# Optimization experiments

Measured on AMD Instinct MI355X. Metric: run time of the kernel, lower is better.

## Reference

```python
import jax, jax.numpy as jnp
import numpy as np

ALPHA = 0.2  # LeakyReLU negative slope
NEG_INF = -1.0e9

def gat_layer(h, adj_mask, W, a, concat):
    # h: [B,N,Fin], W: [Fout,Fin] (torch Linear layout), a: [2*Fout]
    Wh = jnp.einsum('bni,oi->bno', h, W)  # [B,N,Fout]
    F_out = W.shape[0]
    # a([Wh_i, Wh_j]) = Wh_i . a[:F] + Wh_j . a[F:]  (avoids O(N^2*2F) concat, same math)
    s_src = Wh @ a[:F_out]  # [B,N]
    s_dst = Wh @ a[F_out:]  # [B,N]
    e = jax.nn.leaky_relu(s_src[:, :, None] + s_dst[:, None, :], ALPHA)  # [B,N,N]
    e = jnp.where(adj_mask, e, NEG_INF)
    att = jax.nn.softmax(e, axis=-1)  # dropout is identity in eval mode
    h_prime = jnp.einsum('bij,bjf->bif', att, Wh)
    return jax.nn.elu(h_prime) if concat else h_prime

def setup_inputs() -> dict:
    key = jax.random.key(0)
    ks = jax.random.split(key, 8)
    B, N = 4, 2048
    IN, HID, OUT, H = 64, 64, 32, 4
    x = jax.random.normal(ks[0], (B, N, IN), dtype=jnp.float32)
    adj = jax.random.randint(ks[1], (B, N, N), 0, 2, dtype=jnp.int32)

    def xavier(k, shape):
        fan_out, fan_in = shape[0], shape[1]
        lim = float(np.sqrt(6.0 / (fan_in + fan_out)))
        return jax.random.uniform(k, shape, jnp.float32, -lim, lim)

    W1 = jnp.stack([xavier(jax.random.fold_in(ks[2], i), (HID, IN)) for i in range(H)])      # [H,64,64]
    a1 = jnp.stack([xavier(jax.random.fold_in(ks[3], i), (1, 2 * HID))[0] for i in range(H)])  # [H,128]
    W2 = xavier(ks[4], (OUT, H * HID))  # [32,256]
    a2 = xavier(ks[5], (1, 2 * OUT))[0]  # [64]
    return {"x": x, "adj": adj, "W1": W1, "a1": a1, "W2": W2, "a2": a2}

def reference(x, adj, W1, a1, W2, a2):
    mask = adj > 0
    # layer 1: num_heads concat heads with ELU
    heads = [gat_layer(x, mask, W1[k], a1[k], True) for k in range(W1.shape[0])]
    h = jnp.concatenate(heads, axis=-1)  # [B,N,H*HID]
    # output layer: single head, no ELU
    return gat_layer(h, mask, W2, a2, False)
```

## Files before the change

### kernel.cpp

```cpp
#include <hip/hip_runtime.h>
#include <hip/hip_bf16.h>
#include <cstdint>

#define NN 2048
#define NH 4
#define NW 64

typedef __attribute__((ext_vector_type(8))) short bf16x8;
typedef __attribute__((ext_vector_type(4))) float f32x4;
typedef __attribute__((ext_vector_type(4))) int i32x4;
typedef __attribute__((ext_vector_type(4))) unsigned short u16x4;

__device__ __forceinline__ float lrelu(float s) { return s > 0.f ? s : 0.2f * s; }

__device__ __forceinline__ unsigned pk2(float lo, float hi) {
  __hip_bfloat162 h2 = __float22bfloat162_rn(make_float2(lo, hi));
  union { __hip_bfloat162 h; unsigned u; } c; c.h = h2; return c.u;
}
__device__ __forceinline__ unsigned short f2bf1(float f) {
  __hip_bfloat16 h = __float2bfloat16(f);
  union { __hip_bfloat16 h; unsigned short u; } c; c.h = h; return c.u;
}
__device__ __forceinline__ bf16x8 cvt8(f32x4 v0, f32x4 v1) {
  union { unsigned u[4]; bf16x8 v; } r;
  r.u[0] = pk2(v0[0], v0[1]); r.u[1] = pk2(v0[2], v0[3]);
  r.u[2] = pk2(v1[0], v1[1]); r.u[3] = pk2(v1[2], v1[3]);
  return r.v;
}


__global__ __launch_bounds__(256) void kA(
    const int* __restrict__ adj, unsigned* __restrict__ mb,
    const float* __restrict__ x, const float* __restrict__ W1,
    const float* __restrict__ a1, unsigned short* __restrict__ wht1,
    float* __restrict__ ssrc1, float* __restrict__ G1g, float* __restrict__ G2g) {
  if (blockIdx.x >= 512) {
    size_t gid = (size_t)(blockIdx.x - 512) * 256 + threadIdx.x;
    const i32x4* ap = (const i32x4*)adj + gid * 8;
    i32x4 v0 = __builtin_nontemporal_load(ap + 0);
    i32x4 v1 = __builtin_nontemporal_load(ap + 1);
    i32x4 v2 = __builtin_nontemporal_load(ap + 2);
    i32x4 v3 = __builtin_nontemporal_load(ap + 3);
    i32x4 v4 = __builtin_nontemporal_load(ap + 4);
    i32x4 v5 = __builtin_nontemporal_load(ap + 5);
    i32x4 v6 = __builtin_nontemporal_load(ap + 6);
    i32x4 v7 = __builtin_nontemporal_load(ap + 7);
    unsigned word = 0;
#pragma unroll
    for (int j = 0; j < 4; ++j) {
      word |= ((unsigned)(v0[j] != 0)) << (0 + j);
      word |= ((unsigned)(v1[j] != 0)) << (4 + j);
      word |= ((unsigned)(v2[j] != 0)) << (8 + j);
      word |= ((unsigned)(v3[j] != 0)) << (12 + j);
      word |= ((unsigned)(v4[j] != 0)) << (16 + j);
      word |= ((unsigned)(v5[j] != 0)) << (20 + j);
      word |= ((unsigned)(v6[j] != 0)) << (24 + j);
      word |= ((unsigned)(v7[j] != 0)) << (28 + j);
    }
    mb[gid] = word;
    return;
  }
  int blk = blockIdx.x;
  int rowg = blk * 16;
  int b = rowg >> 11, rloc = rowg & (NN - 1);
  int tid = threadIdx.x, lane = tid & 63, h = tid >> 6;
  int cl = lane & 15, g = lane >> 4;

  const float* xr = x + (size_t)(rowg + cl) * 64 + 8 * g;
  bf16x8 af[2];
#pragma unroll
  for (int ks = 0; ks < 2; ++ks)
    af[ks] = cvt8(*(const f32x4*)(xr + ks * 32), *(const f32x4*)(xr + ks * 32 + 4));

  f32x4 zero = {0.f, 0.f, 0.f, 0.f};
  f32x4 acc[4] = {zero, zero, zero, zero};
#pragma unroll
  for (int ft = 0; ft < 4; ++ft) {
    const float* wr = W1 + (size_t)(h * 64 + ft * 16 + cl) * 64 + 8 * g;
#pragma unroll
    for (int ks = 0; ks < 2; ++ks) {
      bf16x8 bfr = cvt8(*(const f32x4*)(wr + ks * 32), *(const f32x4*)(wr + ks * 32 + 4));
      acc[ft] = __builtin_amdgcn_mfma_f32_16x16x32_bf16(af[ks], bfr, acc[ft], 0, 0, 0);
    }
  }
  unsigned short* bhb = wht1 + (size_t)(b * NH + h) * 64 * NN;
  int kb = rloc >> 5;
  int gd = ((rloc >> 3) & 2) + (g >> 1);
  int e0 = 4 * (g & 1);
  float ps[4] = {0.f, 0.f, 0.f, 0.f}, pd[4] = {0.f, 0.f, 0.f, 0.f};
#pragma unroll
  for (int ft = 0; ft < 4; ++ft) {
    float as = a1[h * 128 + ft * 16 + cl];
    float ad = a1[h * 128 + 64 + ft * 16 + cl];
    u16x4 w4;
#pragma unroll
    for (int r = 0; r < 4; ++r) {
      float v = acc[ft][r];
      w4[r] = f2bf1(v);
      ps[r] += v * as; pd[r] += v * ad;
    }
    *(u16x4*)(bhb + (size_t)(kb * 4 + ft) * 512 + cl * 8 + gd * 128 + e0) = w4;
  }
#pragma unroll
  for (int r = 0; r < 4; ++r) {
    float s = ps[r], d = pd[r];
    s += __shfl_xor(s, 1); s += __shfl_xor(s, 2); s += __shfl_xor(s, 4); s += __shfl_xor(s, 8);
    d += __shfl_xor(d, 1); d += __shfl_xor(d, 2); d += __shfl_xor(d, 4); d += __shfl_xor(d, 8);
    if (cl == 0) {
      int idx = (b * NH + h) * NN + rloc + 4 * g + r;
      ssrc1[idx] = s;
      G1g[idx] = __expf(d);
      G2g[idx] = __expf(0.2f * d);
    }
  }
}

__global__ __launch_bounds__(512) void k2_attn1(
    const unsigned short* __restrict__ wht1, const float* __restrict__ ssrc1,
    const float* __restrict__ G1g, const float* __restrict__ G2g,
    const unsigned* __restrict__ mb, unsigned short* __restrict__ hout) {
  __shared__ __align__(16) char smem[33280];
  __shared__ float swmax[8];
  unsigned (*sdm)[65] = (unsigned(*)[65])smem;
  float* sG1 = (float*)(smem + 16640);
  float* sG2 = (float*)(smem + 16640 + 8192);
  float (*cmb)[16][68] = (float(*)[16][68])smem;
  float (*sden)[16] = (float(*)[16])(smem + 17408);

  int bid = blockIdx.x;
  int bh = bid & 15, tile = bid >> 4;
  int b = bh >> 2, h = bh & 3;
  int rowblk = tile << 6;
  int t = threadIdx.x, lane = t & 63, w = t >> 6;
  int wloc = w & 3, jh = w >> 2;
  int cl = lane & 15, g = lane >> 4, g8 = g * 8;

  {
    int row = t >> 3, c = (t & 7) * 8;
    const unsigned* mrow = mb + (size_t)(b * NN + rowblk + row) * NW + c;
    uint4 v0 = *(const uint4*)(mrow);
    uint4 v1 = *(const uint4*)(mrow + 4);
    sdm[row][c + 0] = v0.x; sdm[row][c + 1] = v0.y;
    sdm[row][c + 2] = v0.z; sdm[row][c + 3] = v0.w;
    sdm[row][c + 4] = v1.x; sdm[row][c + 5] = v1.y;
    sdm[row][c + 6] = v1.z; sdm[row][c + 7] = v1.w;
  }
  {
    const f32x4* g1p = (const f32x4*)(G1g + (size_t)(b * NH + h) * NN);
    const f32x4* g2p = (const f32x4*)(G2g + (size_t)(b * NH + h) * NN);
    f32x4 gv = g1p[t];
    ((f32x4*)sG1)[t] = gv;
    ((f32x4*)sG2)[t] = g2p[t];
    float gmx = fmaxf(fmaxf(gv[0], gv[1]), fmaxf(gv[2], gv[3]));
    gmx = fmaxf(gmx, __shfl_xor(gmx, 1));  gmx = fmaxf(gmx, __shfl_xor(gmx, 2));
    gmx = fmaxf(gmx, __shfl_xor(gmx, 4));  gmx = fmaxf(gmx, __shfl_xor(gmx, 8));
    gmx = fmaxf(gmx, __shfl_xor(gmx, 16)); gmx = fmaxf(gmx, __shfl_xor(gmx, 32));
    if (lane == 0) swmax[w] = gmx;
  }
  int rowW = rowblk + wloc * 16;
  float s = ssrc1[(size_t)(b * NH + h) * NN + rowW + cl];
  __syncthreads();
  float mxv = fmaxf(fmaxf(fmaxf(swmax[0], swmax[1]), fmaxf(swmax[2], swmax[3])),
                    fmaxf(fmaxf(swmax[4], swmax[5]), fmaxf(swmax[6], swmax[7])));
  float logMx = __logf(mxv);
  float m = lrelu(s + logMx);
  float F1 = __expf(s - m), F2 = __expf(0.2f * s - m);

  short onev = (cl == 0) ? (short)0x3F80 : (short)0;
  bf16x8 ones = {onev, onev, onev, onev, onev, onev, onev, onev};
  f32x4 zero = {0.f, 0.f, 0.f, 0.f};
  f32x4 acc[4] = {zero, zero, zero, zero};
  f32x4 acc1 = zero;
  const unsigned short* fbase = wht1 + (size_t)(b * NH + h) * 64 * NN + lane * 8;
  int rloc = wloc * 16 + cl;
  int kb0 = jh * 32;

  bf16x8 curf[4], nxtf[4];
#pragma unroll
  for (int ft = 0; ft < 4; ++ft)
    curf[ft] = *(const bf16x8*)(fbase + (size_t)(kb0 * 4 + ft) * 512);

  for (int i = 0; i < 32; ++i) {
    int kb = kb0 + i;
    if (i < 31) {
#pragma unroll
      for (int ft = 0; ft < 4; ++ft)
        nxtf[ft] = *(const bf16x8*)(fbase + (size_t)((kb + 1) * 4 + ft) * 512);
    }
    unsigned by = (sdm[rloc][kb] >> g8) & 0xFFu;
    int j0 = kb * 32 + g8;
    f32x4 g1a = *(const f32x4*)(sG1 + j0);
    f32x4 g1b = *(const f32x4*)(sG1 + j0 + 4);
    f32x4 g2a = *(const f32x4*)(sG2 + j0);
    f32x4 g2b = *(const f32x4*)(sG2 + j0 + 4);
    float wv[8];
#pragma unroll
    for (int e = 0; e < 8; ++e) {
      float g1 = (e < 4) ? g1a[e] : g1b[e - 4];
      float g2 = (e < 4) ? g2a[e] : g2b[e - 4];
      float v = fmaxf(F1 * g1, F2 * g2);
      wv[e] = ((by >> e) & 1u) ? v : 0.f;
    }
    union { unsigned u[4]; bf16x8 v; } pa;
    pa.u[0] = pk2(wv[0], wv[1]); pa.u[1] = pk2(wv[2], wv[3]);
    pa.u[2] = pk2(wv[4], wv[5]); pa.u[3] = pk2(wv[6], wv[7]);
#pragma unroll
    for (int ft = 0; ft < 4; ++ft)
      acc[ft] = __builtin_amdgcn_mfma_f32_16x16x32_bf16(pa.v, curf[ft], acc[ft], 0, 0, 0);
    acc1 = __builtin_amdgcn_mfma_f32_16x16x32_bf16(pa.v, ones, acc1, 0, 0, 0);
#pragma unroll
    for (int ft = 0; ft < 4; ++ft) curf[ft] = nxtf[ft];
  }
  __syncthreads();
  if (jh == 1) {
#pragma unroll
    for (int ft = 0; ft < 4; ++ft)
#pragma unroll
      for (int r = 0; r < 4; ++r)
        cmb[wloc][4 * g + r][ft * 16 + cl] = acc[ft][r];
    if (cl == 0) {
#pragma unroll
      for (int r = 0; r < 4; ++r) sden[wloc][4 * g + r] = acc1[r];
    }
  }
  __syncthreads();
  if (jh == 0) {
#pragma unroll
    for (int r = 0; r < 4; ++r) {
      int rowm = 4 * g + r;
      float dself = __shfl(acc1[r], lane & 48);
      float inv = 1.f / (dself + sden[wloc][rowm]);
      unsigned short* dst = hout + (size_t)(b * NN + rowW + rowm) * 256 + h * 64;
#pragma unroll
      for (int ft = 0; ft < 4; ++ft) {
        float v = (acc[ft][r] + cmb[wloc][rowm][ft * 16 + cl]) * inv;
        v = v > 0.f ? v : (__expf(v) - 1.f);
        dst[ft * 16 + cl] = f2bf1(v);
      }
    }
  }
}

__global__ __launch_bounds__(256) void k3_proj2(
    const unsigned short* __restrict__ hin, const float* __restrict__ W2,
    const float* __restrict__ a2, unsigned short* __restrict__ wh2t,
    float* __restrict__ ssrc2, float* __restrict__ G1o, float* __restrict__ G2o) {
  __shared__ float cmb[4][16][33];
  int blk = blockIdx.x;
  int b = blk >> 7, rowbase = (blk & 127) << 4;
  int t = threadIdx.x, lane = t & 63, w = t >> 6;
  int cl = lane & 15, g = lane >> 4;
  int k0 = w * 64;

  const unsigned short* hr = hin + (size_t)(b * NN + rowbase + cl) * 256 + k0 + 8 * g;
  bf16x8 af[2];
#pragma unroll
  for (int ks = 0; ks < 2; ++ks)
    af[ks] = *(const bf16x8*)(hr + ks * 32);

  f32x4 zero = {0.f, 0.f, 0.f, 0.f};
  f32x4 acc[2] = {zero, zero};
#pragma unroll
  for (int ft = 0; ft < 2; ++ft) {
    const float* wr = W2 + (size_t)(ft * 16 + cl) * 256 + k0 + 8 * g;
#pragma unroll
    for (int ks = 0; ks < 2; ++ks) {
      bf16x8 bfr = cvt8(*(const f32x4*)(wr + ks * 32), *(const f32x4*)(wr + ks * 32 + 4));
      acc[ft] = __builtin_amdgcn_mfma_f32_16x16x32_bf16(af[ks], bfr, acc[ft], 0, 0, 0);
    }
  }
#pragma unroll
  for (int ft = 0; ft < 2; ++ft)
#pragma unroll
    for (int r = 0; r < 4; ++r)
      cmb[w][4 * g + r][ft * 16 + cl] = acc[ft][r];
  __syncthreads();

  int row = t >> 4, c0 = t & 15;
  float v0 = cmb[0][row][c0] + cmb[1][row][c0] + cmb[2][row][c0] + cmb[3][row][c0];
  float v1 = cmb[0][row][c0 + 16] + cmb[1][row][c0 + 16] + cmb[2][row][c0 + 16] + cmb[3][row][c0 + 16];
  float ps = v0 * a2[c0] + v1 * a2[c0 + 16];
  float pd = v0 * a2[32 + c0] + v1 * a2[32 + c0 + 16];
  ps += __shfl_xor(ps, 1); ps += __shfl_xor(ps, 2); ps += __shfl_xor(ps, 4); ps += __shfl_xor(ps, 8);
  pd += __shfl_xor(pd, 1); pd += __shfl_xor(pd, 2); pd += __shfl_xor(pd, 4); pd += __shfl_xor(pd, 8);
  if (c0 == 0) {
    int idx = b * NN + rowbase + row;
    ssrc2[idx] = ps;
    G1o[idx] = __expf(pd);
    G2o[idx] = __expf(0.2f * pd);
  }
  cmb[0][row][c0] = v0;
  cmb[0][row][c0 + 16] = v1;
  __syncthreads();
  int col = t >> 3, rg = t & 7;
  unsigned pk = pk2(cmb[0][2 * rg][col], cmb[0][2 * rg + 1][col]);
  int kb2 = rowbase >> 5;
  int gd = ((rowbase >> 3) & 2) + (rg >> 2);
  size_t off = (size_t)(kb2 * 2 + (col >> 4)) * 512 + (col & 15) * 8 + gd * 128 + 2 * (rg & 3);
  *(unsigned*)(wh2t + (size_t)b * 32 * NN + off) = pk;
}

__global__ __launch_bounds__(512) void k4_attn2(
    const unsigned short* __restrict__ wh2t, const float* __restrict__ ssrc2,
    const float* __restrict__ G1o, const float* __restrict__ G2o,
    const unsigned* __restrict__ mb, float* __restrict__ outp) {
  __shared__ __align__(16) char smem[24704];
  __shared__ float swmax[8];
  unsigned (*sdm)[65] = (unsigned(*)[65])smem;
  float* sG1 = (float*)(smem + 8320);
  float* sG2 = (float*)(smem + 8320 + 8192);
  float (*cmb)[2][16][36] = (float(*)[2][16][36])smem;
  float (*sden)[2][16] = (float(*)[2][16])(smem + 13824);

  int bid = blockIdx.x;
  int b = bid & 3, tile = bid >> 2;
  int rowblk = tile << 5;
  int t = threadIdx.x, lane = t & 63, w = t >> 6;
  int wloc = w & 1, jh = w >> 1;
  int cl = lane & 15, g = lane >> 4, g8 = g * 8;

  {
    int row = t >> 4, c = (t & 15) * 4;
    uint4 v = *(const uint4*)(mb + (size_t)(b * NN + rowblk + row) * NW + c);
    sdm[row][c + 0] = v.x; sdm[row][c + 1] = v.y;
    sdm[row][c + 2] = v.z; sdm[row][c + 3] = v.w;
  }
  {
    f32x4 gv = ((const f32x4*)(G1o + (size_t)b * NN))[t];
    ((f32x4*)sG1)[t] = gv;
    ((f32x4*)sG2)[t] = ((const f32x4*)(G2o + (size_t)b * NN))[t];
    float gmx = fmaxf(fmaxf(gv[0], gv[1]), fmaxf(gv[2], gv[3]));
    gmx = fmaxf(gmx, __shfl_xor(gmx, 1));  gmx = fmaxf(gmx, __shfl_xor(gmx, 2));
    gmx = fmaxf(gmx, __shfl_xor(gmx, 4));  gmx = fmaxf(gmx, __shfl_xor(gmx, 8));
    gmx = fmaxf(gmx, __shfl_xor(gmx, 16)); gmx = fmaxf(gmx, __shfl_xor(gmx, 32));
    if (lane == 0) swmax[w] = gmx;
  }
  int rowW = rowblk + wloc * 16;
  float s = ssrc2[b * NN + rowW + cl];
  __syncthreads();
  float mxv = fmaxf(fmaxf(fmaxf(swmax[0], swmax[1]), fmaxf(swmax[2], swmax[3])),
                    fmaxf(fmaxf(swmax[4], swmax[5]), fmaxf(swmax[6], swmax[7])));
  float logMx = __logf(mxv);
  float m = lrelu(s + logMx);
  float F1 = __expf(s - m), F2 = __expf(0.2f * s - m);

  short onev = (cl == 0) ? (short)0x3F80 : (short)0;
  bf16x8 ones = {onev, onev, onev, onev, onev, onev, onev, onev};
  f32x4 zero = {0.f, 0.f, 0.f, 0.f};
  f32x4 acc[2] = {zero, zero};
  f32x4 acc1 = zero;
  const unsigned short* fbase = wh2t + (size_t)b * 32 * NN + lane * 8;
  int rloc = wloc * 16 + cl;
  int kb0 = jh * 16;

  bf16x8 curf[2], nxtf[2];
#pragma unroll
  for (int ft = 0; ft < 2; ++ft)
    curf[ft] = *(const bf16x8*)(fbase + (size_t)(kb0 * 2 + ft) * 512);

  for (int i = 0; i < 16; ++i) {
    int kb = kb0 + i;
    if (i < 15) {
#pragma unroll
      for (int ft = 0; ft < 2; ++ft)
        nxtf[ft] = *(const bf16x8*)(fbase + (size_t)((kb + 1) * 2 + ft) * 512);
    }
    unsigned by = (sdm[rloc][kb] >> g8) & 0xFFu;
    int j0 = kb * 32 + g8;
    f32x4 g1a = *(const f32x4*)(sG1 + j0);
    f32x4 g1b = *(const f32x4*)(sG1 + j0 + 4);
    f32x4 g2a = *(const f32x4*)(sG2 + j0);
    f32x4 g2b = *(const f32x4*)(sG2 + j0 + 4);
    float wv[8];
#pragma unroll
    for (int e = 0; e < 8; ++e) {
      float g1 = (e < 4) ? g1a[e] : g1b[e - 4];
      float g2 = (e < 4) ? g2a[e] : g2b[e - 4];
      float v = fmaxf(F1 * g1, F2 * g2);
      wv[e] = ((by >> e) & 1u) ? v : 0.f;
    }
    union { unsigned u[4]; bf16x8 v; } pa;
    pa.u[0] = pk2(wv[0], wv[1]); pa.u[1] = pk2(wv[2], wv[3]);
    pa.u[2] = pk2(wv[4], wv[5]); pa.u[3] = pk2(wv[6], wv[7]);
#pragma unroll
    for (int ft = 0; ft < 2; ++ft)
      acc[ft] = __builtin_amdgcn_mfma_f32_16x16x32_bf16(pa.v, curf[ft], acc[ft], 0, 0, 0);
    acc1 = __builtin_amdgcn_mfma_f32_16x16x32_bf16(pa.v, ones, acc1, 0, 0, 0);
#pragma unroll
    for (int ft = 0; ft < 2; ++ft) curf[ft] = nxtf[ft];
  }
  __syncthreads();
  if (jh > 0) {
#pragma unroll
    for (int ft = 0; ft < 2; ++ft)
#pragma unroll
      for (int r = 0; r < 4; ++r)
        cmb[jh - 1][wloc][4 * g + r][ft * 16 + cl] = acc[ft][r];
    if (cl == 0) {
#pragma unroll
      for (int r = 0; r < 4; ++r) sden[jh - 1][wloc][4 * g + r] = acc1[r];
    }
  }
  __syncthreads();
  if (jh == 0) {
#pragma unroll
    for (int r = 0; r < 4; ++r) {
      int rowm = 4 * g + r;
      float dself = __shfl(acc1[r], lane & 48);
      float den = dself + sden[0][wloc][rowm] + sden[1][wloc][rowm] + sden[2][wloc][rowm];
      float inv = 1.f / den;
      float* dst = outp + (size_t)(b * NN + rowW + rowm) * 32;
#pragma unroll
      for (int ft = 0; ft < 2; ++ft) {
        float v = acc[ft][r] + cmb[0][wloc][rowm][ft * 16 + cl] +
                  cmb[1][wloc][rowm][ft * 16 + cl] + cmb[2][wloc][rowm][ft * 16 + cl];
        dst[ft * 16 + cl] = v * inv;
      }
    }
  }
}

extern "C" void kernel_launch(void* const* d_in, const int* in_sizes, int n_in,
                              void* d_out, int out_size, void* d_ws, size_t ws_size,
                              hipStream_t stream) {
  (void)in_sizes; (void)n_in; (void)out_size; (void)ws_size;
  const float* x   = (const float*)d_in[0];
  const int*   adj = (const int*)d_in[1];
  const float* W1  = (const float*)d_in[2];
  const float* a1  = (const float*)d_in[3];
  const float* W2  = (const float*)d_in[4];
  const float* a2  = (const float*)d_in[5];
  float* outp = (float*)d_out;
  char* ws = (char*)d_ws;

  unsigned*       mbits = (unsigned*)(ws);
  unsigned short* wht1  = (unsigned short*)(ws + (size_t)(2u << 20));
  float*          ssrc1 = (float*)(ws + (size_t)(6u << 20));
  float*          G1g   = (float*)(ws + (size_t)(6u << 20) + (128u << 10));
  float*          G2g   = (float*)(ws + (size_t)(6u << 20) + (256u << 10));
  unsigned short* hbuf  = (unsigned short*)(ws + (size_t)(6u << 20) + (512u << 10));
  unsigned short* wh2t  = (unsigned short*)(ws + (size_t)(14u << 20) + (512u << 10));
  float*          ssrc2 = (float*)(ws + (size_t)(15u << 20));
  float*          G1o   = (float*)(ws + (size_t)(15u << 20) + (32u << 10));
  float*          G2o   = (float*)(ws + (size_t)(15u << 20) + (64u << 10));

  kA      <<<2560, 256, 0, stream>>>(adj, mbits, x, W1, a1, wht1, ssrc1, G1g, G2g);
  k2_attn1<<<512,  512, 0, stream>>>(wht1, ssrc1, G1g, G2g, mbits, hbuf);
  k3_proj2<<<512,  256, 0, stream>>>(hbuf, W2, a2, wh2t, ssrc2, G1o, G2o);
  k4_attn2<<<256,  512, 0, stream>>>(wh2t, ssrc2, G1o, G2o, mbits, outp);
}
```

Measured before the change: 165.9 us.

## Reorganize attn1 warps to 2 row-tiles x 4 K-splits, reusing B fragments

The layer-1 attention kernel now assigns each wave 32 rows (two 16-row MFMA tiles) and splits the neighbour dimension four ways instead of two. Each loaded Wh fragment therefore feeds two MFMAs, halving the global B-operand traffic per wave and shortening each wave's loop. The cost is a larger shared buffer for reducing three partial accumulators, more registers per wave, and a launch_bounds occupancy hint of 4 blocks. The larger LDS footprint may limit how many blocks fit per CU.

```diff
diff --git a/kernel.cpp b/kernel.cpp
--- a/kernel.cpp
+++ b/kernel.cpp
@@ -115,25 +115,26 @@
   }
 }
 
-__global__ __launch_bounds__(512) void k2_attn1(
+__global__ __launch_bounds__(512, 4) void k2_attn1(
     const unsigned short* __restrict__ wht1, const float* __restrict__ ssrc1,
     const float* __restrict__ G1g, const float* __restrict__ G2g,
     const unsigned* __restrict__ mb, unsigned short* __restrict__ hout) {
-  __shared__ __align__(16) char smem[33280];
+  __shared__ __align__(16) char smem[53248];
   __shared__ float swmax[8];
   unsigned (*sdm)[65] = (unsigned(*)[65])smem;
   float* sG1 = (float*)(smem + 16640);
   float* sG2 = (float*)(smem + 16640 + 8192);
-  float (*cmb)[16][68] = (float(*)[16][68])smem;
-  float (*sden)[16] = (float(*)[16])(smem + 17408);
+  float (*cmb)[2][32][68] = (float(*)[2][32][68])smem;
+  float (*sden)[2][32] = (float(*)[2][32])(smem + 52224);
 
   int bid = blockIdx.x;
   int bh = bid & 15, tile = bid >> 4;
   int b = bh >> 2, h = bh & 3;
   int rowblk = tile << 6;
   int t = threadIdx.x, lane = t & 63, w = t >> 6;
-  int wloc = w & 3, jh = w >> 2;
+  int rt = w & 1, jh = w >> 1;
   int cl = lane & 15, g = lane >> 4, g8 = g * 8;
+  int rbase = rt * 32;
 
   {
     int row = t >> 3, c = (t & 7) * 8;
@@ -157,85 +158,105 @@
     gmx = fmaxf(gmx, __shfl_xor(gmx, 16)); gmx = fmaxf(gmx, __shfl_xor(gmx, 32));
     if (lane == 0) swmax[w] = gmx;
   }
-  int rowW = rowblk + wloc * 16;
-  float s = ssrc1[(size_t)(b * NH + h) * NN + rowW + cl];
+  size_t sbase = (size_t)(b * NH + h) * NN + rowblk + rbase;
+  float s0 = ssrc1[sbase + cl];
+  float s1 = ssrc1[sbase + 16 + cl];
   __syncthreads();
   float mxv = fmaxf(fmaxf(fmaxf(swmax[0], swmax[1]), fmaxf(swmax[2], swmax[3])),
                     fmaxf(fmaxf(swmax[4], swmax[5]), fmaxf(swmax[6], swmax[7])));
   float logMx = __logf(mxv);
-  float m = lrelu(s + logMx);
-  float F1 = __expf(s - m), F2 = __expf(0.2f * s - m);
+  float m0 = lrelu(s0 + logMx), m1 = lrelu(s1 + logMx);
+  float F10 = __expf(s0 - m0), F20 = __expf(0.2f * s0 - m0);
+  float F11 = __expf(s1 - m1), F21 = __expf(0.2f * s1 - m1);
 
   short onev = (cl == 0) ? (short)0x3F80 : (short)0;
   bf16x8 ones = {onev, onev, onev, onev, onev, onev, onev, onev};
   f32x4 zero = {0.f, 0.f, 0.f, 0.f};
-  f32x4 acc[4] = {zero, zero, zero, zero};
-  f32x4 acc1 = zero;
+  f32x4 acc[2][4] = {{zero, zero, zero, zero}, {zero, zero, zero, zero}};
+  f32x4 accd[2] = {zero, zero};
   const unsigned short* fbase = wht1 + (size_t)(b * NH + h) * 64 * NN + lane * 8;
-  int rloc = wloc * 16 + cl;
-  int kb0 = jh * 32;
+  int kb0 = jh * 16;
 
   bf16x8 curf[4], nxtf[4];
 #pragma unroll
   for (int ft = 0; ft < 4; ++ft)
     curf[ft] = *(const bf16x8*)(fbase + (size_t)(kb0 * 4 + ft) * 512);
 
-  for (int i = 0; i < 32; ++i) {
+  for (int i = 0; i < 16; ++i) {
     int kb = kb0 + i;
-    if (i < 31) {
+    if (i < 15) {
 #pragma unroll
       for (int ft = 0; ft < 4; ++ft)
         nxtf[ft] = *(const bf16x8*)(fbase + (size_t)((kb + 1) * 4 + ft) * 512);
     }
-    unsigned by = (sdm[rloc][kb] >> g8) & 0xFFu;
+    unsigned by0 = (sdm[rbase + cl][kb] >> g8) & 0xFFu;
+    unsigned by1 = (sdm[rbase + 16 + cl][kb] >> g8) & 0xFFu;
     int j0 = kb * 32 + g8;
     f32x4 g1a = *(const f32x4*)(sG1 + j0);
     f32x4 g1b = *(const f32x4*)(sG1 + j0 + 4);
     f32x4 g2a = *(const f32x4*)(sG2 + j0);
     f32x4 g2b = *(const f32x4*)(sG2 + j0 + 4);
-    float wv[8];
+    float wv0[8], wv1[8];
 #pragma unroll
     for (int e = 0; e < 8; ++e) {
       float g1 = (e < 4) ? g1a[e] : g1b[e - 4];
       float g2 = (e < 4) ? g2a[e] : g2b[e - 4];
-      float v = fmaxf(F1 * g1, F2 * g2);
-      wv[e] = ((by >> e) & 1u) ? v : 0.f;
-    }
-    union { unsigned u[4]; bf16x8 v; } pa;
-    pa.u[0] = pk2(wv[0], wv[1]); pa.u[1] = pk2(wv[2], wv[3]);
-    pa.u[2] = pk2(wv[4], wv[5]); pa.u[3] = pk2(wv[6], wv[7]);
-#pragma unroll
-    for (int ft = 0; ft < 4; ++ft)
-      acc[ft] = __builtin_amdgcn_mfma_f32_16x16x32_bf16(pa.v, curf[ft], acc[ft], 0, 0, 0);
-    acc1 = __builtin_amdgcn_mfma_f32_16x16x32_bf16(pa.v, ones, acc1, 0, 0, 0);
+      float v0 = fmaxf(F10 * g1, F20 * g2);
+      float v1 = fmaxf(F11 * g1, F21 * g2);
+      wv0[e] = ((by0 >> e) & 1u) ? v0 : 0.f;
+      wv1[e] = ((by1 >> e) & 1u) ? v1 : 0.f;
+    }
+    union { unsigned u[4]; bf16x8 v; } pa0, pa1;
+    pa0.u[0] = pk2(wv0[0], wv0[1]); pa0.u[1] = pk2(wv0[2], wv0[3]);
+    pa0.u[2] = pk2(wv0[4], wv0[5]); pa0.u[3] = pk2(wv0[6], wv0[7]);
+    pa1.u[0] = pk2(wv1[0], wv1[1]); pa1.u[1] = pk2(wv1[2], wv1[3]);
+    pa1.u[2] = pk2(wv1[4], wv1[5]); pa1.u[3] = pk2(wv1[6], wv1[7]);
+#pragma unroll
+    for (int ft = 0; ft < 4; ++ft) {
+      acc[0][ft] = __builtin_amdgcn_mfma_f32_16x16x32_bf16(pa0.v, curf[ft], acc[0][ft], 0, 0, 0);
+      acc[1][ft] = __builtin_amdgcn_mfma_f32_16x16x32_bf16(pa1.v, curf[ft], acc[1][ft], 0, 0, 0);
+    }
+    accd[0] = __builtin_amdgcn_mfma_f32_16x16x32_bf16(pa0.v, ones, accd[0], 0, 0, 0);
+    accd[1] = __builtin_amdgcn_mfma_f32_16x16x32_bf16(pa1.v, ones, accd[1], 0, 0, 0);
 #pragma unroll
     for (int ft = 0; ft < 4; ++ft) curf[ft] = nxtf[ft];
   }
   __syncthreads();
-  if (jh == 1) {
-#pragma unroll
-    for (int ft = 0; ft < 4; ++ft)
-#pragma unroll
-      for (int r = 0; r < 4; ++r)
-        cmb[wloc][4 * g + r][ft * 16 + cl] = acc[ft][r];
-    if (cl == 0) {
-#pragma unroll
-      for (int r = 0; r < 4; ++r) sden[wloc][4 * g + r] = acc1[r];
+  if (jh > 0) {
+    int p = jh - 1;
+#pragma unroll
+    for (int f = 0; f < 2; ++f) {
+#pragma unroll
+      for (int ft = 0; ft < 4; ++ft)
+#pragma unroll
+        for (int r = 0; r < 4; ++r)
+          cmb[p][rt][f * 16 + 4 * g + r][ft * 16 + cl] = acc[f][ft][r];
+      if (cl == 0) {
+#pragma unroll
+        for (int r = 0; r < 4; ++r) sden[p][rt][f * 16 + 4 * g + r] = accd[f][r];
+      }
     }
   }
   __syncthreads();
   if (jh == 0) {
 #pragma unroll
-    for (int r = 0; r < 4; ++r) {
-      int rowm = 4 * g + r;
-      float dself = __shfl(acc1[r], lane & 48);
-      float inv = 1.f / (dself + sden[wloc][rowm]);
-      unsigned short* dst = hout + (size_t)(b * NN + rowW + rowm) * 256 + h * 64;
-#pragma unroll
-      for (int ft = 0; ft < 4; ++ft) {
-        float v = (acc[ft][r] + cmb[wloc][rowm][ft * 16 + cl]) * inv;
-        v = v > 0.f ? v : (__expf(v) - 1.f);
-        dst[ft * 16 + cl] = f2bf1(v);
+    for (int f = 0; f < 2; ++f) {
+#pragma unroll
+      for (int r = 0; r < 4; ++r) {
+        int rloc32 = f * 16 + 4 * g + r;
+        float dself = __shfl(accd[f][r], lane & 48);
+        float den = dself + sden[0][rt][rloc32] + sden[1][rt][rloc32] + sden[2][rt][rloc32];
+        float inv = 1.f / den;
+        int row = rowblk + rbase + rloc32;
+        unsigned short* dst = hout + (size_t)(b * NN + row) * 256 + h * 64;
+#pragma unroll
+        for (int ft = 0; ft < 4; ++ft) {
+          float v = acc[f][ft][r] + cmb[0][rt][rloc32][ft * 16 + cl] +
+                    cmb[1][rt][rloc32][ft * 16 + cl] + cmb[2][rt][rloc32][ft * 16 + cl];
+          v *= inv;
+          v = v > 0.f ? v : (__expf(v) - 1.f);
+          dst[ft * 16 + cl] = f2bf1(v);
+        }
       }
     }
   }
```

New measurement: 164.8 us. Within noise of the previous version (-0.6%).

## Fuse adjacency bitmask packing into layer-1 attention and retile attention kernels

Applied to the files above, without the earlier changes.

Moves the int32 adjacency-to-bitmask conversion out of the projection kernel and into the layer-1 attention kernel. Each block now handles 16 rows for all 4 heads, so the adjacency is read once, packed straight into shared memory, and also written out for layer 2. This avoids writing the bitmask and reading it back within layer 1. Layer-2 attention is retiled to 16 rows per block with 8 waves splitting the key range, which doubles the block count. In exchange, shared memory per layer-1 block grows to about 70KB, which may limit occupancy, and the adjacency read is now serialized before the MFMA loop instead of running concurrently with the projection work.

```diff
diff --git a/kernel.cpp b/kernel.cpp
--- a/kernel.cpp
+++ b/kernel.cpp
@@ -30,36 +30,9 @@
 
 
 __global__ __launch_bounds__(256) void kA(
-    const int* __restrict__ adj, unsigned* __restrict__ mb,
     const float* __restrict__ x, const float* __restrict__ W1,
     const float* __restrict__ a1, unsigned short* __restrict__ wht1,
     float* __restrict__ ssrc1, float* __restrict__ G1g, float* __restrict__ G2g) {
-  if (blockIdx.x >= 512) {
-    size_t gid = (size_t)(blockIdx.x - 512) * 256 + threadIdx.x;
-    const i32x4* ap = (const i32x4*)adj + gid * 8;
-    i32x4 v0 = __builtin_nontemporal_load(ap + 0);
-    i32x4 v1 = __builtin_nontemporal_load(ap + 1);
-    i32x4 v2 = __builtin_nontemporal_load(ap + 2);
-    i32x4 v3 = __builtin_nontemporal_load(ap + 3);
-    i32x4 v4 = __builtin_nontemporal_load(ap + 4);
-    i32x4 v5 = __builtin_nontemporal_load(ap + 5);
-    i32x4 v6 = __builtin_nontemporal_load(ap + 6);
-    i32x4 v7 = __builtin_nontemporal_load(ap + 7);
-    unsigned word = 0;
-#pragma unroll
-    for (int j = 0; j < 4; ++j) {
-      word |= ((unsigned)(v0[j] != 0)) << (0 + j);
-      word |= ((unsigned)(v1[j] != 0)) << (4 + j);
-      word |= ((unsigned)(v2[j] != 0)) << (8 + j);
-      word |= ((unsigned)(v3[j] != 0)) << (12 + j);
-      word |= ((unsigned)(v4[j] != 0)) << (16 + j);
-      word |= ((unsigned)(v5[j] != 0)) << (20 + j);
-      word |= ((unsigned)(v6[j] != 0)) << (24 + j);
-      word |= ((unsigned)(v7[j] != 0)) << (28 + j);
-    }
-    mb[gid] = word;
-    return;
-  }
   int blk = blockIdx.x;
   int rowg = blk * 16;
   int b = rowg >> 11, rloc = rowg & (NN - 1);
@@ -115,53 +88,80 @@
   }
 }
 
-__global__ __launch_bounds__(512) void k2_attn1(
+__global__ __launch_bounds__(512, 4) void k2_attn1(
+    const int* __restrict__ adj, unsigned* __restrict__ mb,
     const unsigned short* __restrict__ wht1, const float* __restrict__ ssrc1,
     const float* __restrict__ G1g, const float* __restrict__ G2g,
-    const unsigned* __restrict__ mb, unsigned short* __restrict__ hout) {
-  __shared__ __align__(16) char smem[33280];
+    unsigned short* __restrict__ hout) {
+  __shared__ __align__(16) char smem[69696];
   __shared__ float swmax[8];
   unsigned (*sdm)[65] = (unsigned(*)[65])smem;
-  float* sG1 = (float*)(smem + 16640);
-  float* sG2 = (float*)(smem + 16640 + 8192);
-  float (*cmb)[16][68] = (float(*)[16][68])smem;
-  float (*sden)[16] = (float(*)[16])(smem + 17408);
+  float* sG1 = (float*)(smem + 4160);
+  float* sG2 = (float*)(smem + 4160 + 32768);
+  float (*cmb)[16][68] = (float(*)[16][68])(smem + 4160);
+  float (*sden)[16] = (float(*)[16])(smem + 4160 + 17408);
 
   int bid = blockIdx.x;
-  int bh = bid & 15, tile = bid >> 4;
-  int b = bh >> 2, h = bh & 3;
-  int rowblk = tile << 6;
+  int b = bid & 3, tile = bid >> 2;
+  int rowblk = tile << 4;
   int t = threadIdx.x, lane = t & 63, w = t >> 6;
-  int wloc = w & 3, jh = w >> 2;
+  int h = w >> 1, jh = w & 1;
   int cl = lane & 15, g = lane >> 4, g8 = g * 8;
 
   {
-    int row = t >> 3, c = (t & 7) * 8;
-    const unsigned* mrow = mb + (size_t)(b * NN + rowblk + row) * NW + c;
-    uint4 v0 = *(const uint4*)(mrow);
-    uint4 v1 = *(const uint4*)(mrow + 4);
-    sdm[row][c + 0] = v0.x; sdm[row][c + 1] = v0.y;
-    sdm[row][c + 2] = v0.z; sdm[row][c + 3] = v0.w;
-    sdm[row][c + 4] = v1.x; sdm[row][c + 5] = v1.y;
-    sdm[row][c + 6] = v1.z; sdm[row][c + 7] = v1.w;
+    int r = t >> 5;
+    int w2 = (t & 31) * 2;
+    const int* arow = adj + ((size_t)(b * NN) + rowblk + r) * NN;
+    unsigned* mrow = mb + ((size_t)(b * NN) + rowblk + r) * NW;
+#pragma unroll
+    for (int k = 0; k < 2; ++k) {
+      int wd = w2 + k;
+      const i32x4* ap = (const i32x4*)(arow + wd * 32);
+      i32x4 v0 = __builtin_nontemporal_load(ap + 0);
+      i32x4 v1 = __builtin_nontemporal_load(ap + 1);
+      i32x4 v2 = __builtin_nontemporal_load(ap + 2);
+      i32x4 v3 = __builtin_nontemporal_load(ap + 3);
+      i32x4 v4 = __builtin_nontemporal_load(ap + 4);
+      i32x4 v5 = __builtin_nontemporal_load(ap + 5);
+      i32x4 v6 = __builtin_nontemporal_load(ap + 6);
+      i32x4 v7 = __builtin_nontemporal_load(ap + 7);
+      unsigned word = 0;
+#pragma unroll
+      for (int j = 0; j < 4; ++j) {
+        word |= ((unsigned)(v0[j] != 0)) << (0 + j);
+        word |= ((unsigned)(v1[j] != 0)) << (4 + j);
+        word |= ((unsigned)(v2[j] != 0)) << (8 + j);
+        word |= ((unsigned)(v3[j] != 0)) << (12 + j);
+        word |= ((unsigned)(v4[j] != 0)) << (16 + j);
+        word |= ((unsigned)(v5[j] != 0)) << (20 + j);
+        word |= ((unsigned)(v6[j] != 0)) << (24 + j);
+        word |= ((unsigned)(v7[j] != 0)) << (28 + j);
+      }
+      sdm[r][wd] = word;
+      mrow[wd] = word;
+    }
   }
   {
-    const f32x4* g1p = (const f32x4*)(G1g + (size_t)(b * NH + h) * NN);
-    const f32x4* g2p = (const f32x4*)(G2g + (size_t)(b * NH + h) * NN);
-    f32x4 gv = g1p[t];
-    ((f32x4*)sG1)[t] = gv;
-    ((f32x4*)sG2)[t] = g2p[t];
-    float gmx = fmaxf(fmaxf(gv[0], gv[1]), fmaxf(gv[2], gv[3]));
+    const f32x4* g1p = (const f32x4*)(G1g + (size_t)(b * NH + h) * NN) + jh * 256;
+    const f32x4* g2p = (const f32x4*)(G2g + (size_t)(b * NH + h) * NN) + jh * 256;
+    f32x4* d1 = (f32x4*)(sG1 + h * NN) + jh * 256;
+    f32x4* d2 = (f32x4*)(sG2 + h * NN) + jh * 256;
+    float gmx = 0.f;
+#pragma unroll
+    for (int it = 0; it < 4; ++it) {
+      f32x4 v = g1p[it * 64 + lane];
+      d1[it * 64 + lane] = v;
+      d2[it * 64 + lane] = g2p[it * 64 + lane];
+      gmx = fmaxf(fmaxf(gmx, v[0]), fmaxf(v[1], fmaxf(v[2], v[3])));
+    }
     gmx = fmaxf(gmx, __shfl_xor(gmx, 1));  gmx = fmaxf(gmx, __shfl_xor(gmx, 2));
     gmx = fmaxf(gmx, __shfl_xor(gmx, 4));  gmx = fmaxf(gmx, __shfl_xor(gmx, 8));
     gmx = fmaxf(gmx, __shfl_xor(gmx, 16)); gmx = fmaxf(gmx, __shfl_xor(gmx, 32));
     if (lane == 0) swmax[w] = gmx;
   }
-  int rowW = rowblk + wloc * 16;
-  float s = ssrc1[(size_t)(b * NH + h) * NN + rowW + cl];
-  __syncthreads();
-  float mxv = fmaxf(fmaxf(fmaxf(swmax[0], swmax[1]), fmaxf(swmax[2], swmax[3])),
-                    fmaxf(fmaxf(swmax[4], swmax[5]), fmaxf(swmax[6], swmax[7])));
+  float s = ssrc1[(size_t)(b * NH + h) * NN + rowblk + cl];
+  __syncthreads();
+  float mxv = fmaxf(swmax[h * 2], swmax[h * 2 + 1]);
   float logMx = __logf(mxv);
   float m = lrelu(s + logMx);
   float F1 = __expf(s - m), F2 = __expf(0.2f * s - m);
@@ -172,7 +172,8 @@
   f32x4 acc[4] = {zero, zero, zero, zero};
   f32x4 acc1 = zero;
   const unsigned short* fbase = wht1 + (size_t)(b * NH + h) * 64 * NN + lane * 8;
-  int rloc = wloc * 16 + cl;
+  const float* gh1 = sG1 + h * NN;
+  const float* gh2 = sG2 + h * NN;
   int kb0 = jh * 32;
 
   bf16x8 curf[4], nxtf[4];
@@ -187,12 +188,12 @@
       for (int ft = 0; ft < 4; ++ft)
         nxtf[ft] = *(const bf16x8*)(fbase + (size_t)((kb + 1) * 4 + ft) * 512);
     }
-    unsigned by = (sdm[rloc][kb] >> g8) & 0xFFu;
+    unsigned by = (sdm[cl][kb] >> g8) & 0xFFu;
     int j0 = kb * 32 + g8;
-    f32x4 g1a = *(const f32x4*)(sG1 + j0);
-    f32x4 g1b = *(const f32x4*)(sG1 + j0 + 4);
-    f32x4 g2a = *(const f32x4*)(sG2 + j0);
-    f32x4 g2b = *(const f32x4*)(sG2 + j0 + 4);
+    f32x4 g1a = *(const f32x4*)(gh1 + j0);
+    f32x4 g1b = *(const f32x4*)(gh1 + j0 + 4);
+    f32x4 g2a = *(const f32x4*)(gh2 + j0);
+    f32x4 g2b = *(const f32x4*)(gh2 + j0 + 4);
     float wv[8];
 #pragma unroll
     for (int e = 0; e < 8; ++e) {
@@ -217,10 +218,10 @@
     for (int ft = 0; ft < 4; ++ft)
 #pragma unroll
       for (int r = 0; r < 4; ++r)
-        cmb[wloc][4 * g + r][ft * 16 + cl] = acc[ft][r];
+        cmb[h][4 * g + r][ft * 16 + cl] = acc[ft][r];
     if (cl == 0) {
 #pragma unroll
-      for (int r = 0; r < 4; ++r) sden[wloc][4 * g + r] = acc1[r];
+      for (int r = 0; r < 4; ++r) sden[h][4 * g + r] = acc1[r];
     }
   }
   __syncthreads();
@@ -229,11 +230,11 @@
     for (int r = 0; r < 4; ++r) {
       int rowm = 4 * g + r;
       float dself = __shfl(acc1[r], lane & 48);
-      float inv = 1.f / (dself + sden[wloc][rowm]);
-      unsigned short* dst = hout + (size_t)(b * NN + rowW + rowm) * 256 + h * 64;
+      float inv = 1.f / (dself + sden[h][rowm]);
+      unsigned short* dst = hout + (size_t)(b * NN + rowblk + rowm) * 256 + h * 64;
 #pragma unroll
       for (int ft = 0; ft < 4; ++ft) {
-        float v = (acc[ft][r] + cmb[wloc][rowm][ft * 16 + cl]) * inv;
+        float v = (acc[ft][r] + cmb[h][rowm][ft * 16 + cl]) * inv;
         v = v > 0.f ? v : (__expf(v) - 1.f);
         dst[ft * 16 + cl] = f2bf1(v);
       }
@@ -304,26 +305,24 @@
     const unsigned short* __restrict__ wh2t, const float* __restrict__ ssrc2,
     const float* __restrict__ G1o, const float* __restrict__ G2o,
     const unsigned* __restrict__ mb, float* __restrict__ outp) {
-  __shared__ __align__(16) char smem[24704];
+  __shared__ __align__(16) char smem[20608];
   __shared__ float swmax[8];
   unsigned (*sdm)[65] = (unsigned(*)[65])smem;
-  float* sG1 = (float*)(smem + 8320);
-  float* sG2 = (float*)(smem + 8320 + 8192);
-  float (*cmb)[2][16][36] = (float(*)[2][16][36])smem;
-  float (*sden)[2][16] = (float(*)[2][16])(smem + 13824);
+  float* sG1 = (float*)(smem + 4160);
+  float* sG2 = (float*)(smem + 4160 + 8192);
+  float (*cmb)[16][36] = (float(*)[16][36])smem;
+  float (*sden)[16] = (float(*)[16])(smem + 16128);
 
   int bid = blockIdx.x;
   int b = bid & 3, tile = bid >> 2;
-  int rowblk = tile << 5;
+  int rowblk = tile << 4;
   int t = threadIdx.x, lane = t & 63, w = t >> 6;
-  int wloc = w & 1, jh = w >> 1;
   int cl = lane & 15, g = lane >> 4, g8 = g * 8;
 
   {
-    int row = t >> 4, c = (t & 15) * 4;
-    uint4 v = *(const uint4*)(mb + (size_t)(b * NN + rowblk + row) * NW + c);
+    int row = t >> 5, c = (t & 31) * 2;
+    uint2 v = *(const uint2*)(mb + (size_t)(b * NN + rowblk + row) * NW + c);
     sdm[row][c + 0] = v.x; sdm[row][c + 1] = v.y;
-    sdm[row][c + 2] = v.z; sdm[row][c + 3] = v.w;
   }
   {
     f32x4 gv = ((const f32x4*)(G1o + (size_t)b * NN))[t];
@@ -335,8 +334,7 @@
     gmx = fmaxf(gmx, __shfl_xor(gmx, 16)); gmx = fmaxf(gmx, __shfl_xor(gmx, 32));
     if (lane == 0) swmax[w] = gmx;
   }
-  int rowW = rowblk + wloc * 16;
-  float s = ssrc2[b * NN + rowW + cl];
+  float s = ssrc2[b * NN + rowblk + cl];
   __syncthreads();
   float mxv = fmaxf(fmaxf(fmaxf(swmax[0], swmax[1]), fmaxf(swmax[2], swmax[3])),
                     fmaxf(fmaxf(swmax[4], swmax[5]), fmaxf(swmax[6], swmax[7])));
@@ -350,22 +348,21 @@
   f32x4 acc[2] = {zero, zero};
   f32x4 acc1 = zero;
   const unsigned short* fbase = wh2t + (size_t)b * 32 * NN + lane * 8;
-  int rloc = wloc * 16 + cl;
-  int kb0 = jh * 16;
+  int kb0 = w * 8;
 
   bf16x8 curf[2], nxtf[2];
 #pragma unroll
   for (int ft = 0; ft < 2; ++ft)
     curf[ft] = *(const bf16x8*)(fbase + (size_t)(kb0 * 2 + ft) * 512);
 
-  for (int i = 0; i < 16; ++i) {
+  for (int i = 0; i < 8; ++i) {
     int kb = kb0 + i;
-    if (i < 15) {
+    if (i < 7) {
 #pragma unroll
       for (int ft = 0; ft < 2; ++ft)
         nxtf[ft] = *(const bf16x8*)(fbase + (size_t)((kb + 1) * 2 + ft) * 512);
     }
-    unsigned by = (sdm[rloc][kb] >> g8) & 0xFFu;
+    unsigned by = (sdm[cl][kb] >> g8) & 0xFFu;
     int j0 = kb * 32 + g8;
     f32x4 g1a = *(const f32x4*)(sG1 + j0);
     f32x4 g1b = *(const f32x4*)(sG1 + j0 + 4);
@@ -390,30 +387,34 @@
     for (int ft = 0; ft < 2; ++ft) curf[ft] = nxtf[ft];
   }
   __syncthreads();
-  if (jh > 0) {
+  if (w > 0) {
+    int p = w - 1;
 #pragma unroll
     for (int ft = 0; ft < 2; ++ft)
 #pragma unroll
       for (int r = 0; r < 4; ++r)
-        cmb[jh - 1][wloc][4 * g + r][ft * 16 + cl] = acc[ft][r];
+        cmb[p][4 * g + r][ft * 16 + cl] = acc[ft][r];
     if (cl == 0) {
 #pragma unroll
-      for (int r = 0; r < 4; ++r) sden[jh - 1][wloc][4 * g + r] = acc1[r];
-    }
-  }
-  __syncthreads();
-  if (jh == 0) {
+      for (int r = 0; r < 4; ++r) sden[p][4 * g + r] = acc1[r];
+    }
+  }
+  __syncthreads();
+  if (w == 0) {
 #pragma unroll
     for (int r = 0; r < 4; ++r) {
       int rowm = 4 * g + r;
       float dself = __shfl(acc1[r], lane & 48);
-      float den = dself + sden[0][wloc][rowm] + sden[1][wloc][rowm] + sden[2][wloc][rowm];
+      float den = dself;
+#pragma unroll
+      for (int p = 0; p < 7; ++p) den += sden[p][rowm];
       float inv = 1.f / den;
-      float* dst = outp + (size_t)(b * NN + rowW + rowm) * 32;
+      float* dst = outp + (size_t)(b * NN + rowblk + rowm) * 32;
 #pragma unroll
       for (int ft = 0; ft < 2; ++ft) {
-        float v = acc[ft][r] + cmb[0][wloc][rowm][ft * 16 + cl] +
-                  cmb[1][wloc][rowm][ft * 16 + cl] + cmb[2][wloc][rowm][ft * 16 + cl];
+        float v = acc[ft][r];
+#pragma unroll
+        for (int p = 0; p < 7; ++p) v += cmb[p][rowm][ft * 16 + cl];
         dst[ft * 16 + cl] = v * inv;
       }
     }
@@ -444,8 +445,8 @@
   float*          G1o   = (float*)(ws + (size_t)(15u << 20) + (32u << 10));
   float*          G2o   = (float*)(ws + (size_t)(15u << 20) + (64u << 10));
 
-  kA      <<<2560, 256, 0, stream>>>(adj, mbits, x, W1, a1, wht1, ssrc1, G1g, G2g);
-  k2_attn1<<<512,  512, 0, stream>>>(wht1, ssrc1, G1g, G2g, mbits, hbuf);
-  k3_proj2<<<512,  256, 0, stream>>>(hbuf, W2, a2, wh2t, ssrc2, G1o, G2o);
-  k4_attn2<<<256,  512, 0, stream>>>(wh2t, ssrc2, G1o, G2o, mbits, outp);
-}
+  kA      <<<512, 256, 0, stream>>>(x, W1, a1, wht1, ssrc1, G1g, G2g);
+  k2_attn1<<<512, 512, 0, stream>>>(adj, mbits, wht1, ssrc1, G1g, G2g, hbuf);
+  k3_proj2<<<512, 256, 0, stream>>>(hbuf, W2, a2, wh2t, ssrc2, G1o, G2o);
+  k4_attn2<<<512, 512, 0, stream>>>(wh2t, ssrc2, G1o, G2o, mbits, outp);
+}
```

Result: slower. 169.4 us (+2.1%).
